# Performance work log

Measured on AMD Instinct MI355X. Metric: run time of the kernel, lower is better.

The kernel has to match this reference:

```python
import jax, jax.numpy as jnp
import numpy as np

H, W_RFFT = 14, 8  # spatial grid 14x14, rfft2 last-dim width = 14//2+1


def setup_inputs() -> dict:
    key = jax.random.key(0)
    k1, k2 = jax.random.split(key)
    B, N, C = 256, 196, 512
    x = jax.random.normal(k1, (B, N, C), dtype=jnp.float32)
    complex_weight = jax.random.normal(k2, (H, W_RFFT, C, 2), dtype=jnp.float32) * 0.02
    return {"x": x, "complex_weight": complex_weight}


def reference(x, complex_weight):
    B, N, C = x.shape
    a = b = int(np.sqrt(N))  # 14
    xg = x.reshape(B, a, b, C).astype(jnp.float32)
    # rfft2 over spatial dims with ortho normalization
    xf = jnp.fft.rfft2(xg, axes=(1, 2), norm="ortho")  # [B, a, b//2+1, C] complex
    weight = complex_weight[..., 0] + 1j * complex_weight[..., 1]  # [a, b//2+1, C]
    xf = xf * weight
    xo = jnp.fft.irfft2(xf, s=(a, b), axes=(1, 2), norm="ortho")  # [B, a, b, C] real
    return xo.astype(x.dtype).reshape(B, N, C)
```

## Files before the change

kernel.cpp:

```cpp
#include <hip/hip_runtime.h>


#define Hs 14
#define Ns 196
#define Cc 512
#define CT 32
#define CONV_THREADS 448

typedef float v2f __attribute__((ext_vector_type(2)));

__global__ __launch_bounds__(256) void prep_a_kernel(const float* __restrict__ cw,
                                                     float* __restrict__ T) {
    __shared__ float cs[14], sn[14];
    if (threadIdx.x < 14) {
        float ang = (float)threadIdx.x * 0.44879895051282760549f;
        cs[threadIdx.x] = cosf(ang);
        sn[threadIdx.x] = sinf(ang);
    }
    __syncthreads();

    int gid = blockIdx.x * 256 + threadIdx.x;
    int c = gid & 511;
    int s = gid >> 9;
    int h = s / 14;
    int dn = s % 14;
    int h2 = (h == 0) ? 0 : (14 - h);

    float Tr = 0.0f, Ti = 0.0f;
    int k = 0;
    #pragma unroll
    for (int w = 0; w < 8; ++w) {
        const float* p = cw + (size_t)(((h * 8 + w) * 512 + c) * 2);
        float Wr = p[0], Wi = p[1];
        Tr += Wr * cs[k] - Wi * sn[k];
        Ti += Wr * sn[k] + Wi * cs[k];
        k += dn; if (k >= 14) k -= 14;
    }
    int k2 = dn; if (k2 >= 14) k2 -= 14;
    #pragma unroll
    for (int w = 1; w < 7; ++w) {
        const float* p = cw + (size_t)(((h2 * 8 + w) * 512 + c) * 2);
        float Wr = p[0], Wi = p[1];
        Tr += Wr * cs[k2] - Wi * sn[k2];
        Ti -= Wr * sn[k2] + Wi * cs[k2];
        k2 += dn; if (k2 >= 14) k2 -= 14;
    }
    float* o = T + (size_t)(s * 512 + c) * 2;
    o[0] = Tr;
    o[1] = Ti;
}

__global__ __launch_bounds__(256) void prep_b_kernel(const float* __restrict__ T,
                                                     float* __restrict__ R) {
    __shared__ float cs[14], sn[14];
    if (threadIdx.x < 14) {
        float ang = (float)threadIdx.x * 0.44879895051282760549f;
        cs[threadIdx.x] = cosf(ang);
        sn[threadIdx.x] = sinf(ang);
    }
    __syncthreads();

    int gid = blockIdx.x * 256 + threadIdx.x;
    int c = gid & 511;
    int s = gid >> 9;
    int dm = s / 14;
    int dn = s % 14;

    float acc = 0.0f;
    int kh = 0;
    #pragma unroll
    for (int h = 0; h < 14; ++h) {
        const float* p = T + (size_t)(((h * 14 + dn) * 512 + c) * 2);
        acc += p[0] * cs[kh] - p[1] * sn[kh];
        kh += dm; if (kh >= 14) kh -= 14;
    }
    R[(size_t)(((dm * 7 + (dn >> 1)) * 512 + c) * 2 + (dn & 1))] = acc * (1.0f / 196.0f);
}

#define SEL_E "op_sel:[0,0,0] op_sel_hi:[1,0,1]"
#define SEL_O "op_sel:[0,1,0] op_sel_hi:[1,1,1]"

#define DIAG(R, S, a0,a1,a2,a3,a4,a5,a6,a7,a8,a9,aA,aB,aC,aD) \
  "v_pk_fma_f32 %" #a0 ", v[40:41], " R ", %" #a0 " " S "\n\t" \
  "v_pk_fma_f32 %" #a1 ", v[42:43], " R ", %" #a1 " " S "\n\t" \
  "v_pk_fma_f32 %" #a2 ", v[44:45], " R ", %" #a2 " " S "\n\t" \
  "v_pk_fma_f32 %" #a3 ", v[46:47], " R ", %" #a3 " " S "\n\t" \
  "v_pk_fma_f32 %" #a4 ", v[48:49], " R ", %" #a4 " " S "\n\t" \
  "v_pk_fma_f32 %" #a5 ", v[50:51], " R ", %" #a5 " " S "\n\t" \
  "v_pk_fma_f32 %" #a6 ", v[52:53], " R ", %" #a6 " " S "\n\t" \
  "v_pk_fma_f32 %" #a7 ", v[54:55], " R ", %" #a7 " " S "\n\t" \
  "v_pk_fma_f32 %" #a8 ", v[56:57], " R ", %" #a8 " " S "\n\t" \
  "v_pk_fma_f32 %" #a9 ", v[58:59], " R ", %" #a9 " " S "\n\t" \
  "v_pk_fma_f32 %" #aA ", v[60:61], " R ", %" #aA " " S "\n\t" \
  "v_pk_fma_f32 %" #aB ", v[62:63], " R ", %" #aB " " S "\n\t" \
  "v_pk_fma_f32 %" #aC ", v[64:65], " R ", %" #aC " " S "\n\t" \
  "v_pk_fma_f32 %" #aD ", v[66:67], " R ", %" #aD " " S "\n\t"

#define XSTRIDE 199
#define RSTRIDE 99

__global__ __launch_bounds__(CONV_THREADS, 2) void conv_kernel(
        const float* __restrict__ x,
        const float* __restrict__ R,
        float* __restrict__ out) {
    __shared__ v2f xs[CT * XSTRIDE];
    __shared__ v2f rs[CT * RSTRIDE];

    const int bx = blockIdx.x;
    const int ct = bx & 15;
    const int bp = bx >> 4;
    const int c0 = ct * CT;
    const int b0 = bp * 2;
    const int t  = threadIdx.x;

    const float* xb = x + (size_t)b0 * Ns * Cc + c0;
    const v2f*  Rbv = (const v2f*)R + c0;
    for (int i = t; i < Ns * CT; i += CONV_THREADS) {
        int pq = i >> 5;
        int cc = i & (CT - 1);
        v2f v;
        v.x = xb[pq * Cc + cc];
        v.y = xb[(size_t)Ns * Cc + pq * Cc + cc];
        xs[cc * XSTRIDE + pq] = v;
    }
    for (int i = t; i < 98 * CT; i += CONV_THREADS) {
        int j  = i >> 5;
        int cc = i & (CT - 1);
        rs[cc * RSTRIDE + j] = Rbv[j * Cc + cc];
    }
    __syncthreads();

    const int c = t & (CT - 1);
    const int m = t >> 5;

    v2f acc[14];
    #pragma unroll
    for (int n = 0; n < 14; ++n) acc[n] = 0.0f;

    const unsigned xs_c = (unsigned)(size_t)&xs[c * XSTRIDE];
    const unsigned rs_c = (unsigned)(size_t)&rs[c * RSTRIDE];

    int dm = m;
    #pragma unroll 1
    for (int p = 0; p < 14; ++p) {
        unsigned xa = xs_c + (unsigned)(p * 14 * 8);
        unsigned ra = rs_c + (unsigned)(dm * 7 * 8);
        asm volatile(
            "ds_read_b64 v[40:41], %14\n\t"
            "ds_read_b64 v[42:43], %14 offset:8\n\t"
            "ds_read_b64 v[44:45], %14 offset:16\n\t"
            "ds_read_b64 v[46:47], %14 offset:24\n\t"
            "ds_read_b64 v[48:49], %14 offset:32\n\t"
            "ds_read_b64 v[50:51], %14 offset:40\n\t"
            "ds_read_b64 v[52:53], %14 offset:48\n\t"
            "ds_read_b64 v[54:55], %14 offset:56\n\t"
            "ds_read_b64 v[56:57], %14 offset:64\n\t"
            "ds_read_b64 v[58:59], %14 offset:72\n\t"
            "ds_read_b64 v[60:61], %14 offset:80\n\t"
            "ds_read_b64 v[62:63], %14 offset:88\n\t"
            "ds_read_b64 v[64:65], %14 offset:96\n\t"
            "ds_read_b64 v[66:67], %14 offset:104\n\t"
            "ds_read_b64 v[68:69], %15\n\t"
            "ds_read_b64 v[70:71], %15 offset:8\n\t"
            "ds_read_b64 v[72:73], %15 offset:16\n\t"
            "ds_read_b64 v[74:75], %15 offset:24\n\t"
            "ds_read_b64 v[76:77], %15 offset:32\n\t"
            "ds_read_b64 v[78:79], %15 offset:40\n\t"
            "ds_read_b64 v[80:81], %15 offset:48\n\t"
            "s_waitcnt lgkmcnt(0)\n\t"
            DIAG("v[68:69]", SEL_E,  0,1,2,3,4,5,6,7,8,9,10,11,12,13)
            DIAG("v[68:69]", SEL_O,  1,2,3,4,5,6,7,8,9,10,11,12,13,0)
            DIAG("v[70:71]", SEL_E,  2,3,4,5,6,7,8,9,10,11,12,13,0,1)
            DIAG("v[70:71]", SEL_O,  3,4,5,6,7,8,9,10,11,12,13,0,1,2)
            DIAG("v[72:73]", SEL_E,  4,5,6,7,8,9,10,11,12,13,0,1,2,3)
            DIAG("v[72:73]", SEL_O,  5,6,7,8,9,10,11,12,13,0,1,2,3,4)
            DIAG("v[74:75]", SEL_E,  6,7,8,9,10,11,12,13,0,1,2,3,4,5)
            DIAG("v[74:75]", SEL_O,  7,8,9,10,11,12,13,0,1,2,3,4,5,6)
            DIAG("v[76:77]", SEL_E,  8,9,10,11,12,13,0,1,2,3,4,5,6,7)
            DIAG("v[76:77]", SEL_O,  9,10,11,12,13,0,1,2,3,4,5,6,7,8)
            DIAG("v[78:79]", SEL_E,  10,11,12,13,0,1,2,3,4,5,6,7,8,9)
            DIAG("v[78:79]", SEL_O,  11,12,13,0,1,2,3,4,5,6,7,8,9,10)
            DIAG("v[80:81]", SEL_E,  12,13,0,1,2,3,4,5,6,7,8,9,10,11)
            DIAG("v[80:81]", SEL_O,  13,0,1,2,3,4,5,6,7,8,9,10,11,12)
            : "+v"(acc[0]), "+v"(acc[1]), "+v"(acc[2]), "+v"(acc[3]),
              "+v"(acc[4]), "+v"(acc[5]), "+v"(acc[6]), "+v"(acc[7]),
              "+v"(acc[8]), "+v"(acc[9]), "+v"(acc[10]), "+v"(acc[11]),
              "+v"(acc[12]), "+v"(acc[13])
            : "v"(xa), "v"(ra)
            : "memory",
              "v40","v41","v42","v43","v44","v45","v46","v47",
              "v48","v49","v50","v51","v52","v53","v54","v55",
              "v56","v57","v58","v59","v60","v61","v62","v63",
              "v64","v65","v66","v67","v68","v69","v70","v71",
              "v72","v73","v74","v75","v76","v77","v78","v79",
              "v80","v81");
        dm = (dm == 0) ? 13 : (dm - 1);
    }

    float* o0 = out + ((size_t)b0 * Ns + m * 14) * Cc + c0 + c;
    float* o1 = o0 + (size_t)Ns * Cc;
    #pragma unroll
    for (int n = 0; n < 14; ++n) {
        o0[n * Cc] = acc[n].x;
        o1[n * Cc] = acc[n].y;
    }
}

extern "C" void kernel_launch(void* const* d_in, const int* in_sizes, int n_in,
                              void* d_out, int out_size, void* d_ws, size_t ws_size,
                              hipStream_t stream) {
    const float* x  = (const float*)d_in[0];
    const float* cw = (const float*)d_in[1];
    float* outp = (float*)d_out;
    float* R = (float*)d_ws;
    float* T = R + (size_t)Ns * Cc;

    prep_a_kernel<<<392, 256, 0, stream>>>(cw, T);
    prep_b_kernel<<<392, 256, 0, stream>>>(T, R);
    conv_kernel<<<128 * 16, CONV_THREADS, 0, stream>>>(x, R, outp);
}
```

Before: 286.9 us.

## Double-buffer LDS reads in conv inner loop with wide b128 loads

The conv loop's inline asm now splits registers into two buffers, A and B. The next iteration's x and R tiles are loaded from LDS while the FMAs for the current tile run, and a trailing s_waitcnt drains the final prefetch. The loads move from 64-bit to 128-bit ds_read, which needs fewer LDS instructions. The launch-bounds occupancy hint rises from 2 to 4 blocks. The risks: more hard-coded VGPRs (up to v125) clash with the higher occupancy target; b128 reads from rows with an odd stride of 199 or 99 float2 may be misaligned; and the per-block LDS footprint cannot fit four blocks per CU anyway.

```diff
diff --git a/kernel.cpp b/kernel.cpp
--- a/kernel.cpp
+++ b/kernel.cpp
@@ -80,7 +80,7 @@
 #define SEL_E "op_sel:[0,0,0] op_sel_hi:[1,0,1]"
 #define SEL_O "op_sel:[0,1,0] op_sel_hi:[1,1,1]"
 
-#define DIAG(R, S, a0,a1,a2,a3,a4,a5,a6,a7,a8,a9,aA,aB,aC,aD) \
+#define DIAG_A(R, S, a0,a1,a2,a3,a4,a5,a6,a7,a8,a9,aA,aB,aC,aD) \
   "v_pk_fma_f32 %" #a0 ", v[40:41], " R ", %" #a0 " " S "\n\t" \
   "v_pk_fma_f32 %" #a1 ", v[42:43], " R ", %" #a1 " " S "\n\t" \
   "v_pk_fma_f32 %" #a2 ", v[44:45], " R ", %" #a2 " " S "\n\t" \
@@ -96,10 +96,103 @@
   "v_pk_fma_f32 %" #aC ", v[64:65], " R ", %" #aC " " S "\n\t" \
   "v_pk_fma_f32 %" #aD ", v[66:67], " R ", %" #aD " " S "\n\t"
 
+#define DIAG_B(R, S, a0,a1,a2,a3,a4,a5,a6,a7,a8,a9,aA,aB,aC,aD) \
+  "v_pk_fma_f32 %" #a0 ", v[68:69], " R ", %" #a0 " " S "\n\t" \
+  "v_pk_fma_f32 %" #a1 ", v[70:71], " R ", %" #a1 " " S "\n\t" \
+  "v_pk_fma_f32 %" #a2 ", v[72:73], " R ", %" #a2 " " S "\n\t" \
+  "v_pk_fma_f32 %" #a3 ", v[74:75], " R ", %" #a3 " " S "\n\t" \
+  "v_pk_fma_f32 %" #a4 ", v[76:77], " R ", %" #a4 " " S "\n\t" \
+  "v_pk_fma_f32 %" #a5 ", v[78:79], " R ", %" #a5 " " S "\n\t" \
+  "v_pk_fma_f32 %" #a6 ", v[80:81], " R ", %" #a6 " " S "\n\t" \
+  "v_pk_fma_f32 %" #a7 ", v[82:83], " R ", %" #a7 " " S "\n\t" \
+  "v_pk_fma_f32 %" #a8 ", v[84:85], " R ", %" #a8 " " S "\n\t" \
+  "v_pk_fma_f32 %" #a9 ", v[86:87], " R ", %" #a9 " " S "\n\t" \
+  "v_pk_fma_f32 %" #aA ", v[88:89], " R ", %" #aA " " S "\n\t" \
+  "v_pk_fma_f32 %" #aB ", v[90:91], " R ", %" #aB " " S "\n\t" \
+  "v_pk_fma_f32 %" #aC ", v[92:93], " R ", %" #aC " " S "\n\t" \
+  "v_pk_fma_f32 %" #aD ", v[94:95], " R ", %" #aD " " S "\n\t"
+
+#define FMAS_A \
+  DIAG_A("v[96:97]",   SEL_E,  0,1,2,3,4,5,6,7,8,9,10,11,12,13) \
+  DIAG_A("v[96:97]",   SEL_O,  1,2,3,4,5,6,7,8,9,10,11,12,13,0) \
+  DIAG_A("v[98:99]",   SEL_E,  2,3,4,5,6,7,8,9,10,11,12,13,0,1) \
+  DIAG_A("v[98:99]",   SEL_O,  3,4,5,6,7,8,9,10,11,12,13,0,1,2) \
+  DIAG_A("v[100:101]", SEL_E,  4,5,6,7,8,9,10,11,12,13,0,1,2,3) \
+  DIAG_A("v[100:101]", SEL_O,  5,6,7,8,9,10,11,12,13,0,1,2,3,4) \
+  DIAG_A("v[102:103]", SEL_E,  6,7,8,9,10,11,12,13,0,1,2,3,4,5) \
+  DIAG_A("v[102:103]", SEL_O,  7,8,9,10,11,12,13,0,1,2,3,4,5,6) \
+  DIAG_A("v[104:105]", SEL_E,  8,9,10,11,12,13,0,1,2,3,4,5,6,7) \
+  DIAG_A("v[104:105]", SEL_O,  9,10,11,12,13,0,1,2,3,4,5,6,7,8) \
+  DIAG_A("v[106:107]", SEL_E,  10,11,12,13,0,1,2,3,4,5,6,7,8,9) \
+  DIAG_A("v[106:107]", SEL_O,  11,12,13,0,1,2,3,4,5,6,7,8,9,10) \
+  DIAG_A("v[108:109]", SEL_E,  12,13,0,1,2,3,4,5,6,7,8,9,10,11) \
+  DIAG_A("v[108:109]", SEL_O,  13,0,1,2,3,4,5,6,7,8,9,10,11,12)
+
+#define FMAS_B \
+  DIAG_B("v[112:113]", SEL_E,  0,1,2,3,4,5,6,7,8,9,10,11,12,13) \
+  DIAG_B("v[112:113]", SEL_O,  1,2,3,4,5,6,7,8,9,10,11,12,13,0) \
+  DIAG_B("v[114:115]", SEL_E,  2,3,4,5,6,7,8,9,10,11,12,13,0,1) \
+  DIAG_B("v[114:115]", SEL_O,  3,4,5,6,7,8,9,10,11,12,13,0,1,2) \
+  DIAG_B("v[116:117]", SEL_E,  4,5,6,7,8,9,10,11,12,13,0,1,2,3) \
+  DIAG_B("v[116:117]", SEL_O,  5,6,7,8,9,10,11,12,13,0,1,2,3,4) \
+  DIAG_B("v[118:119]", SEL_E,  6,7,8,9,10,11,12,13,0,1,2,3,4,5) \
+  DIAG_B("v[118:119]", SEL_O,  7,8,9,10,11,12,13,0,1,2,3,4,5,6) \
+  DIAG_B("v[120:121]", SEL_E,  8,9,10,11,12,13,0,1,2,3,4,5,6,7) \
+  DIAG_B("v[120:121]", SEL_O,  9,10,11,12,13,0,1,2,3,4,5,6,7,8) \
+  DIAG_B("v[122:123]", SEL_E,  10,11,12,13,0,1,2,3,4,5,6,7,8,9) \
+  DIAG_B("v[122:123]", SEL_O,  11,12,13,0,1,2,3,4,5,6,7,8,9,10) \
+  DIAG_B("v[124:125]", SEL_E,  12,13,0,1,2,3,4,5,6,7,8,9,10,11) \
+  DIAG_B("v[124:125]", SEL_O,  13,0,1,2,3,4,5,6,7,8,9,10,11,12)
+
+#define LOADS_TO_A(X, RA) \
+  "ds_read_b128 v[40:43], " X "\n\t" \
+  "ds_read_b128 v[44:47], " X " offset:16\n\t" \
+  "ds_read_b128 v[48:51], " X " offset:32\n\t" \
+  "ds_read_b128 v[52:55], " X " offset:48\n\t" \
+  "ds_read_b128 v[56:59], " X " offset:64\n\t" \
+  "ds_read_b128 v[60:63], " X " offset:80\n\t" \
+  "ds_read_b128 v[64:67], " X " offset:96\n\t" \
+  "ds_read_b128 v[96:99], " RA "\n\t" \
+  "ds_read_b128 v[100:103], " RA " offset:16\n\t" \
+  "ds_read_b128 v[104:107], " RA " offset:32\n\t" \
+  "ds_read_b64  v[108:109], " RA " offset:48\n\t"
+
+#define LOADS_TO_B(X, RA) \
+  "ds_read_b128 v[68:71], " X "\n\t" \
+  "ds_read_b128 v[72:75], " X " offset:16\n\t" \
+  "ds_read_b128 v[76:79], " X " offset:32\n\t" \
+  "ds_read_b128 v[80:83], " X " offset:48\n\t" \
+  "ds_read_b128 v[84:87], " X " offset:64\n\t" \
+  "ds_read_b128 v[88:91], " X " offset:80\n\t" \
+  "ds_read_b128 v[92:95], " X " offset:96\n\t" \
+  "ds_read_b128 v[112:115], " RA "\n\t" \
+  "ds_read_b128 v[116:119], " RA " offset:16\n\t" \
+  "ds_read_b128 v[120:123], " RA " offset:32\n\t" \
+  "ds_read_b64  v[124:125], " RA " offset:48\n\t"
+
+#define CLOB \
+  "v40","v41","v42","v43","v44","v45","v46","v47", \
+  "v48","v49","v50","v51","v52","v53","v54","v55", \
+  "v56","v57","v58","v59","v60","v61","v62","v63", \
+  "v64","v65","v66","v67","v68","v69","v70","v71", \
+  "v72","v73","v74","v75","v76","v77","v78","v79", \
+  "v80","v81","v82","v83","v84","v85","v86","v87", \
+  "v88","v89","v90","v91","v92","v93","v94","v95", \
+  "v96","v97","v98","v99","v100","v101","v102","v103", \
+  "v104","v105","v106","v107","v108","v109", \
+  "v112","v113","v114","v115","v116","v117","v118","v119", \
+  "v120","v121","v122","v123","v124","v125"
+
+#define ACCS \
+  "+v"(acc[0]), "+v"(acc[1]), "+v"(acc[2]), "+v"(acc[3]), \
+  "+v"(acc[4]), "+v"(acc[5]), "+v"(acc[6]), "+v"(acc[7]), \
+  "+v"(acc[8]), "+v"(acc[9]), "+v"(acc[10]), "+v"(acc[11]), \
+  "+v"(acc[12]), "+v"(acc[13])
+
 #define XSTRIDE 199
 #define RSTRIDE 99
 
-__global__ __launch_bounds__(CONV_THREADS, 2) void conv_kernel(
+__global__ __launch_bounds__(CONV_THREADS, 4) void conv_kernel(
         const float* __restrict__ x,
         const float* __restrict__ R,
         float* __restrict__ out) {
@@ -140,62 +233,37 @@
     const unsigned xs_c = (unsigned)(size_t)&xs[c * XSTRIDE];
     const unsigned rs_c = (unsigned)(size_t)&rs[c * RSTRIDE];
 
+    {
+        unsigned xa = xs_c;
+        unsigned ra = rs_c + (unsigned)(m * 56);
+        asm volatile(LOADS_TO_A("%0", "%1")
+                     : : "v"(xa), "v"(ra) : "memory", CLOB);
+    }
+
     int dm = m;
     #pragma unroll 1
-    for (int p = 0; p < 14; ++p) {
-        unsigned xa = xs_c + (unsigned)(p * 14 * 8);
-        unsigned ra = rs_c + (unsigned)(dm * 7 * 8);
+    for (int pp = 0; pp < 7; ++pp) {
+        int p = 2 * pp;
+        dm = (dm == 0) ? 13 : (dm - 1);
+        unsigned xb1 = xs_c + (unsigned)((p + 1) * 112);
+        unsigned rb1 = rs_c + (unsigned)(dm * 56);
         asm volatile(
-            "ds_read_b64 v[40:41], %14\n\t"
-            "ds_read_b64 v[42:43], %14 offset:8\n\t"
-            "ds_read_b64 v[44:45], %14 offset:16\n\t"
-            "ds_read_b64 v[46:47], %14 offset:24\n\t"
-            "ds_read_b64 v[48:49], %14 offset:32\n\t"
-            "ds_read_b64 v[50:51], %14 offset:40\n\t"
-            "ds_read_b64 v[52:53], %14 offset:48\n\t"
-            "ds_read_b64 v[54:55], %14 offset:56\n\t"
-            "ds_read_b64 v[56:57], %14 offset:64\n\t"
-            "ds_read_b64 v[58:59], %14 offset:72\n\t"
-            "ds_read_b64 v[60:61], %14 offset:80\n\t"
-            "ds_read_b64 v[62:63], %14 offset:88\n\t"
-            "ds_read_b64 v[64:65], %14 offset:96\n\t"
-            "ds_read_b64 v[66:67], %14 offset:104\n\t"
-            "ds_read_b64 v[68:69], %15\n\t"
-            "ds_read_b64 v[70:71], %15 offset:8\n\t"
-            "ds_read_b64 v[72:73], %15 offset:16\n\t"
-            "ds_read_b64 v[74:75], %15 offset:24\n\t"
-            "ds_read_b64 v[76:77], %15 offset:32\n\t"
-            "ds_read_b64 v[78:79], %15 offset:40\n\t"
-            "ds_read_b64 v[80:81], %15 offset:48\n\t"
             "s_waitcnt lgkmcnt(0)\n\t"
-            DIAG("v[68:69]", SEL_E,  0,1,2,3,4,5,6,7,8,9,10,11,12,13)
-            DIAG("v[68:69]", SEL_O,  1,2,3,4,5,6,7,8,9,10,11,12,13,0)
-            DIAG("v[70:71]", SEL_E,  2,3,4,5,6,7,8,9,10,11,12,13,0,1)
-            DIAG("v[70:71]", SEL_O,  3,4,5,6,7,8,9,10,11,12,13,0,1,2)
-            DIAG("v[72:73]", SEL_E,  4,5,6,7,8,9,10,11,12,13,0,1,2,3)
-            DIAG("v[72:73]", SEL_O,  5,6,7,8,9,10,11,12,13,0,1,2,3,4)
-            DIAG("v[74:75]", SEL_E,  6,7,8,9,10,11,12,13,0,1,2,3,4,5)
-            DIAG("v[74:75]", SEL_O,  7,8,9,10,11,12,13,0,1,2,3,4,5,6)
-            DIAG("v[76:77]", SEL_E,  8,9,10,11,12,13,0,1,2,3,4,5,6,7)
-            DIAG("v[76:77]", SEL_O,  9,10,11,12,13,0,1,2,3,4,5,6,7,8)
-            DIAG("v[78:79]", SEL_E,  10,11,12,13,0,1,2,3,4,5,6,7,8,9)
-            DIAG("v[78:79]", SEL_O,  11,12,13,0,1,2,3,4,5,6,7,8,9,10)
-            DIAG("v[80:81]", SEL_E,  12,13,0,1,2,3,4,5,6,7,8,9,10,11)
-            DIAG("v[80:81]", SEL_O,  13,0,1,2,3,4,5,6,7,8,9,10,11,12)
-            : "+v"(acc[0]), "+v"(acc[1]), "+v"(acc[2]), "+v"(acc[3]),
-              "+v"(acc[4]), "+v"(acc[5]), "+v"(acc[6]), "+v"(acc[7]),
-              "+v"(acc[8]), "+v"(acc[9]), "+v"(acc[10]), "+v"(acc[11]),
-              "+v"(acc[12]), "+v"(acc[13])
-            : "v"(xa), "v"(ra)
-            : "memory",
-              "v40","v41","v42","v43","v44","v45","v46","v47",
-              "v48","v49","v50","v51","v52","v53","v54","v55",
-              "v56","v57","v58","v59","v60","v61","v62","v63",
-              "v64","v65","v66","v67","v68","v69","v70","v71",
-              "v72","v73","v74","v75","v76","v77","v78","v79",
-              "v80","v81");
+            LOADS_TO_B("%14", "%15")
+            FMAS_A
+            : ACCS : "v"(xb1), "v"(rb1) : "memory", CLOB);
+
         dm = (dm == 0) ? 13 : (dm - 1);
-    }
+        int p2 = (p + 2 == 14) ? 0 : (p + 2);
+        unsigned xa2 = xs_c + (unsigned)(p2 * 112);
+        unsigned ra2 = rs_c + (unsigned)(dm * 56);
+        asm volatile(
+            "s_waitcnt lgkmcnt(0)\n\t"
+            LOADS_TO_A("%14", "%15")
+            FMAS_B
+            : ACCS : "v"(xa2), "v"(ra2) : "memory", CLOB);
+    }
+    asm volatile("s_waitcnt lgkmcnt(0)" ::: "memory");
 
     float* o0 = out + ((size_t)b0 * Ns + m * 14) * Cc + c0 + c;
     float* o1 = o0 + (size_t)Ns * Cc;
```

After: 404.5 us. 41.0% more time.
